# Performance work log

Measured on AMD Instinct MI355X. Metric: run time of the kernel, lower is better.

## Reference

```python
import jax, jax.numpy as jnp
import numpy as np

OUTPUT_SIZE = 512


def _build_schedule(n, m):
    """Static pyramid-circuit schedule of Givens/RBS gates on n wires.

    Sequential gate order (matches theta ordering): for k = 1..n-1, apply
    gates on adjacent wire pairs (i, i+1) for i = k-1 down to max(k-m, 0).
    Total gates = (2n - m - 1) * m // 2. Gates are packed into a brickwork
    schedule (timestep t = 2(k-1) - i) so each layer touches disjoint pairs
    and the whole chain runs in T = n + m - 2 parallel layers.
    Padded slots point at dummy wires (n, n+1) and are masked to identity.
    """
    layers = {}
    t_idx = 0
    for k in range(1, n):
        for i in range(k - 1, max(k - m, 0) - 1, -1):
            t = 2 * (k - 1) - i
            layers.setdefault(t, []).append((i, t_idx))
            t_idx += 1
    T = max(layers) + 1
    W = max(len(v) for v in layers.values())
    wire = np.full((T, W), n, dtype=np.int32)   # pad gates hit dummy wires (n, n+1)
    tidx = np.zeros((T, W), dtype=np.int32)
    mask = np.zeros((T, W), dtype=np.float32)
    for t, gs in layers.items():
        for j, (i, ti) in enumerate(gs):
            wire[t, j] = i
            tidx[t, j] = ti
            mask[t, j] = 1.0
    return wire, tidx, mask


def apply_orthogonal(thetas, x, output_size):
    input_size = x.shape[-1]
    n, m = max(input_size, output_size), min(input_size, output_size)
    wire, tidx, mask = _build_schedule(n, m)
    if input_size < n:
        x = jnp.pad(x, ((0, 0), (0, n - input_size)))
    state = jnp.pad(x, ((0, 0), (0, 2)))          # two dummy columns for padded gate slots
    th = thetas[jnp.asarray(tidx)]                # [T, W]
    msk = jnp.asarray(mask)
    cos = jnp.where(msk > 0, jnp.cos(th), 1.0)    # padded slots -> identity rotation
    sin = jnp.where(msk > 0, jnp.sin(th), 0.0)
    wa = jnp.asarray(wire)                        # [T, W] first wire of each pair
    wb = wa + 1

    def step(st, layer):
        c, s, a_idx, b_idx = layer
        a = st[:, a_idx]                          # [B, W]
        b = st[:, b_idx]
        st = st.at[:, a_idx].set(c * a + s * b)   # RBS rotation on each pair
        st = st.at[:, b_idx].set(c * b - s * a)
        return st, None

    state, _ = jax.lax.scan(step, state, (cos, sin, wa, wb))
    return state[:, :output_size]


def setup_inputs():
    key = jax.random.key(0)
    k1, k2 = jax.random.split(key)
    B, N = 256, 512
    n_thetas = (2 * max(N, OUTPUT_SIZE) - min(N, OUTPUT_SIZE) - 1) * min(N, OUTPUT_SIZE) // 2
    x = jax.random.normal(k1, (B, N), dtype=jnp.float32)
    thetas = jax.random.uniform(k2, (n_thetas,), dtype=jnp.float32,
                                minval=-np.pi, maxval=np.pi)
    bias = jnp.zeros((OUTPUT_SIZE,), dtype=jnp.float32)
    return {"x": x, "thetas": thetas, "bias": bias}


def reference(x, thetas, bias):
    # normalize_inputs=False path; with_bias=True
    out = apply_orthogonal(thetas, x, OUTPUT_SIZE)
    return out + bias
```

## Files before the change

### kernel.cpp

```cpp
#include <hip/hip_runtime.h>
#include <hip/hip_fp16.h>
#include <stdint.h>


#define N_WIRES 512
#define BATCH   256
#define PAIRS   510
#define PF      10
#define FINAL4  (PAIRS * 128)
#define TOTAL4  (FINAL4 + 64)
#define TOTALH2 (TOTAL4 * 4)

__global__ __launch_bounds__(256) void fused_kernel(
    const float* __restrict__ thetas, __half2* __restrict__ Wh) {
  int tid = blockIdx.x * 256 + threadIdx.x;
  if (tid >= TOTALH2) return;
  float c = 1.0f, s = 0.0f;
  if (tid < PAIRS * 512) {
    int p = tid >> 9, r = tid & 511;
    int h = r >> 8, rr = r & 255, L = rr >> 2, j = rr & 3;
    int t = 2 * p + h;
    int i = 8 * L + 2 * j + h;
    if (i <= min(t, 1020 - t)) {
      int k = ((t + i) >> 1) + 1;
      int idx = ((k * (k - 1)) >> 1) + (k - 1 - i);
      __sincosf(thetas[idx], &s, &c);
    }
    if (h == 1 && j == 3) c -= 1.0f;
  } else {
    int e = tid - PAIRS * 512;
    int L = e >> 2, j = e & 3;
    if (8 * L + 2 * j == 0) __sincosf(thetas[130815], &s, &c);
  }
  Wh[tid] = __floats2half2_rn(c, s);
}

template <int N>
__device__ __forceinline__ void wait_vm() {
  asm volatile("s_waitcnt vmcnt(%0)" ::"i"(N) : "memory");
}

__device__ __forceinline__ float dpp_shr1(float v) {
  return __int_as_float(
      __builtin_amdgcn_mov_dpp(__float_as_int(v), 0x138, 0xF, 0xF, true));
}
__device__ __forceinline__ float dpp_shl1(float v) {
  return __int_as_float(
      __builtin_amdgcn_mov_dpp(__float_as_int(v), 0x130, 0xF, 0xF, true));
}
__device__ __forceinline__ uint32_t dpp_shr1_u(uint32_t v) {
  return (uint32_t)__builtin_amdgcn_mov_dpp((int)v, 0x138, 0xF, 0xF, true);
}

__device__ __forceinline__ float mix_s(uint32_t g, float b) {
  float d;
  asm("v_fma_mix_f32 %0, %1, %2, 0 op_sel:[1,0,0] op_sel_hi:[1,0,0]"
      : "=v"(d)
      : "v"(g), "v"(b));
  return d;
}
__device__ __forceinline__ float mix_ns(uint32_t g, float b) {
  float d;
  asm("v_fma_mix_f32 %0, -%1, %2, 0 op_sel:[1,0,0] op_sel_hi:[1,0,0]"
      : "=v"(d)
      : "v"(g), "v"(b));
  return d;
}
__device__ __forceinline__ float mix_c_acc(uint32_t g, float b, float acc) {
  float d;
  asm("v_fma_mix_f32 %0, %1, %2, %3 op_sel:[0,0,0] op_sel_hi:[1,0,0]"
      : "=v"(d)
      : "v"(g), "v"(b), "v"(acc));
  return d;
}

__device__ __forceinline__ void gate_mix(float& a, float& b, uint32_t g) {
  float t = mix_s(g, b);
  float u = mix_ns(g, a);
  float na = mix_c_acc(g, a, t);
  float nb = mix_c_acc(g, b, u);
  a = na;
  b = nb;
}

__device__ __forceinline__ void pair_compute(float& v0, float& v1, float& v2,
                                             float& v3, float& v4, float& v5,
                                             float& v6, float& v7,
                                             const uint4& E, const uint4& O) {
  gate_mix(v0, v1, E.x);
  gate_mix(v2, v3, E.y);
  gate_mix(v4, v5, E.z);
  gate_mix(v6, v7, E.w);
  uint32_t bl = dpp_shr1_u(O.w);
  float rv0 = dpp_shl1(v0);
  float lv7 = dpp_shr1(v7);
  gate_mix(v1, v2, O.x);
  gate_mix(v3, v4, O.y);
  gate_mix(v5, v6, O.z);
  float t = mix_s(O.w, rv0);
  t = mix_c_acc(O.w, v7, t);
  v7 = t + v7;
  float u = mix_ns(bl, lv7);
  u = mix_c_acc(bl, v0, u);
  v0 = u + v0;
}

__global__ __launch_bounds__(64, 1) void circuit_kernel(
    const float* __restrict__ x, const uint32_t* __restrict__ W,
    const float* __restrict__ bias, float* __restrict__ out) {
  const int lane = threadIdx.x;
  const int row = blockIdx.x;
  const uint4* __restrict__ Wg = (const uint4*)W;

  uint4 R[PF][2];
  const uint4* pw = Wg + lane;
#pragma unroll
  for (int s = 0; s < PF; ++s) {
    R[s][0] = pw[0];
    R[s][1] = pw[64];
    pw += 128;
  }

  const float* xr = x + row * N_WIRES + lane * 8;
  float4 x0 = *(const float4*)(xr);
  float4 x1 = *(const float4*)(xr + 4);
  float v0 = x0.x, v1 = x0.y, v2 = x0.z, v3 = x0.w;
  float v4 = x1.x, v5 = x1.y, v6 = x1.z, v7 = x1.w;

  for (int blk = 0; blk < (PAIRS / PF) - 1; ++blk) {
#pragma unroll
    for (int s = 0; s < PF; ++s) {
      wait_vm<18>();
      pair_compute(v0, v1, v2, v3, v4, v5, v6, v7, R[s][0], R[s][1]);
      R[s][0] = pw[0];
      R[s][1] = pw[64];
      pw += 128;
    }
  }

  wait_vm<0>();
#pragma unroll
  for (int s = 0; s < PF; ++s)
    pair_compute(v0, v1, v2, v3, v4, v5, v6, v7, R[s][0], R[s][1]);

  uint4 F = Wg[FINAL4 + lane];
  gate_mix(v0, v1, F.x);
  gate_mix(v2, v3, F.y);
  gate_mix(v4, v5, F.z);
  gate_mix(v6, v7, F.w);

  const float* br = bias + lane * 8;
  float4 b0 = *(const float4*)(br);
  float4 b1 = *(const float4*)(br + 4);
  float* orow = out + row * N_WIRES + lane * 8;
  float4 o0 = {v0 + b0.x, v1 + b0.y, v2 + b0.z, v3 + b0.w};
  float4 o1 = {v4 + b1.x, v5 + b1.y, v6 + b1.z, v7 + b1.w};
  *(float4*)(orow) = o0;
  *(float4*)(orow + 4) = o1;
}

extern "C" void kernel_launch(void* const* d_in, const int* in_sizes, int n_in,
                              void* d_out, int out_size, void* d_ws,
                              size_t ws_size, hipStream_t stream) {
  const float* x = (const float*)d_in[0];
  const float* thetas = (const float*)d_in[1];
  const float* bias = (const float*)d_in[2];
  float* out = (float*)d_out;

  uint32_t* W = (uint32_t*)d_ws;

  fused_kernel<<<(TOTALH2 + 255) / 256, 256, 0, stream>>>(thetas, (__half2*)W);
  circuit_kernel<<<BATCH, 64, 0, stream>>>(x, W, bias, out);
}
```

Measured before the change: 115.5 us.

## Compose gate windows into banded fp16 matrices and apply via MFMA

The per-row sequential simulation of all gate layers is replaced with a two-stage scheme. A window kernel propagates basis vectors through each block of 57 layer-pairs, producing nine banded 512x512 fp16 transfer matrices. The apply kernel then multiplies batches of 16 rows by these matrices with MFMA, using only the three diagonal 64-wide blocks, and ping-pongs the activations in shared memory. This trades the long serial dependency chain for more total arithmetic, converts activations to fp16 (a precision risk), and runs the apply stage on only 16 blocks.

```diff
diff --git a/kernel.cpp b/kernel.cpp
--- a/kernel.cpp
+++ b/kernel.cpp
@@ -3,35 +3,30 @@
 #include <stdint.h>
 
 
-#define N_WIRES 512
-#define BATCH   256
-#define PAIRS   510
-#define PF      10
-#define FINAL4  (PAIRS * 128)
-#define TOTAL4  (FINAL4 + 64)
-#define TOTALH2 (TOTAL4 * 4)
+#define PAIRS   511
+#define TOTALH2 (PAIRS * 512)
+#define NWIN    9
+#define WPAIRS  57
+#define VT_ELEMS (512 * 512)
+#define VT_OFF_BYTES 1048576
+
+typedef _Float16 half8_t __attribute__((ext_vector_type(8)));
+typedef float f32x4_t __attribute__((ext_vector_type(4)));
 
 __global__ __launch_bounds__(256) void fused_kernel(
     const float* __restrict__ thetas, __half2* __restrict__ Wh) {
   int tid = blockIdx.x * 256 + threadIdx.x;
-  if (tid >= TOTALH2) return;
+  int p = tid >> 9, r = tid & 511;
+  int h = r >> 8, rr = r & 255, L = rr >> 2, j = rr & 3;
+  int t = 2 * p + h;
+  int i = 8 * L + 2 * j + h;
   float c = 1.0f, s = 0.0f;
-  if (tid < PAIRS * 512) {
-    int p = tid >> 9, r = tid & 511;
-    int h = r >> 8, rr = r & 255, L = rr >> 2, j = rr & 3;
-    int t = 2 * p + h;
-    int i = 8 * L + 2 * j + h;
-    if (i <= min(t, 1020 - t)) {
-      int k = ((t + i) >> 1) + 1;
-      int idx = ((k * (k - 1)) >> 1) + (k - 1 - i);
-      __sincosf(thetas[idx], &s, &c);
-    }
-    if (h == 1 && j == 3) c -= 1.0f;
-  } else {
-    int e = tid - PAIRS * 512;
-    int L = e >> 2, j = e & 3;
-    if (8 * L + 2 * j == 0) __sincosf(thetas[130815], &s, &c);
-  }
+  if (i <= min(t, 1020 - t)) {
+    int k = ((t + i) >> 1) + 1;
+    int idx = ((k * (k - 1)) >> 1) + (k - 1 - i);
+    __sincosf(thetas[idx], &s, &c);
+  }
+  if (h == 1 && j == 3) c -= 1.0f;
   Wh[tid] = __floats2half2_rn(c, s);
 }
 
@@ -39,41 +34,33 @@
 __device__ __forceinline__ void wait_vm() {
   asm volatile("s_waitcnt vmcnt(%0)" ::"i"(N) : "memory");
 }
-
-__device__ __forceinline__ float dpp_shr1(float v) {
+template <int CTRL>
+__device__ __forceinline__ float dpp_f(float v) {
   return __int_as_float(
-      __builtin_amdgcn_mov_dpp(__float_as_int(v), 0x138, 0xF, 0xF, true));
-}
-__device__ __forceinline__ float dpp_shl1(float v) {
-  return __int_as_float(
-      __builtin_amdgcn_mov_dpp(__float_as_int(v), 0x130, 0xF, 0xF, true));
-}
-__device__ __forceinline__ uint32_t dpp_shr1_u(uint32_t v) {
-  return (uint32_t)__builtin_amdgcn_mov_dpp((int)v, 0x138, 0xF, 0xF, true);
-}
-
+      __builtin_amdgcn_mov_dpp(__float_as_int(v), CTRL, 0xF, 0xF, true));
+}
+template <int CTRL>
+__device__ __forceinline__ uint32_t dpp_u(uint32_t v) {
+  return (uint32_t)__builtin_amdgcn_mov_dpp((int)v, CTRL, 0xF, 0xF, true);
+}
 __device__ __forceinline__ float mix_s(uint32_t g, float b) {
   float d;
   asm("v_fma_mix_f32 %0, %1, %2, 0 op_sel:[1,0,0] op_sel_hi:[1,0,0]"
-      : "=v"(d)
-      : "v"(g), "v"(b));
+      : "=v"(d) : "v"(g), "v"(b));
   return d;
 }
 __device__ __forceinline__ float mix_ns(uint32_t g, float b) {
   float d;
   asm("v_fma_mix_f32 %0, -%1, %2, 0 op_sel:[1,0,0] op_sel_hi:[1,0,0]"
-      : "=v"(d)
-      : "v"(g), "v"(b));
+      : "=v"(d) : "v"(g), "v"(b));
   return d;
 }
 __device__ __forceinline__ float mix_c_acc(uint32_t g, float b, float acc) {
   float d;
   asm("v_fma_mix_f32 %0, %1, %2, %3 op_sel:[0,0,0] op_sel_hi:[1,0,0]"
-      : "=v"(d)
-      : "v"(g), "v"(b), "v"(acc));
+      : "=v"(d) : "v"(g), "v"(b), "v"(acc));
   return d;
 }
-
 __device__ __forceinline__ void gate_mix(float& a, float& b, uint32_t g) {
   float t = mix_s(g, b);
   float u = mix_ns(g, a);
@@ -83,6 +70,7 @@
   b = nb;
 }
 
+template <int CSHL, int CSHR>
 __device__ __forceinline__ void pair_compute(float& v0, float& v1, float& v2,
                                              float& v3, float& v4, float& v5,
                                              float& v6, float& v7,
@@ -91,9 +79,9 @@
   gate_mix(v2, v3, E.y);
   gate_mix(v4, v5, E.z);
   gate_mix(v6, v7, E.w);
-  uint32_t bl = dpp_shr1_u(O.w);
-  float rv0 = dpp_shl1(v0);
-  float lv7 = dpp_shr1(v7);
+  uint32_t bl = dpp_u<CSHR>(O.w);
+  float rv0 = dpp_f<CSHL>(v0);
+  float lv7 = dpp_f<CSHR>(v7);
   gate_mix(v1, v2, O.x);
   gate_mix(v3, v4, O.y);
   gate_mix(v5, v6, O.z);
@@ -105,58 +93,144 @@
   v0 = u + v0;
 }
 
-__global__ __launch_bounds__(64, 1) void circuit_kernel(
-    const float* __restrict__ x, const uint32_t* __restrict__ W,
+__global__ __launch_bounds__(64) void window_kernel(
+    const uint32_t* __restrict__ W, _Float16* __restrict__ VT) {
+  const int lane = threadIdx.x;
+  const int gl = lane & 15, grp = lane >> 4;
+  const int w = blockIdx.x >> 7;
+  const int d = ((blockIdx.x & 127) << 2) + grp;
+  int b0 = d - 58;
+  int base = (b0 <= 0) ? 0 : (b0 & ~7);
+  base = min(base, 384);
+  const int idx0 = (base >> 3) + gl;
+  const int wire0 = base + 8 * gl;
+
+  float v0 = (wire0 + 0 == d) ? 1.f : 0.f;
+  float v1 = (wire0 + 1 == d) ? 1.f : 0.f;
+  float v2 = (wire0 + 2 == d) ? 1.f : 0.f;
+  float v3 = (wire0 + 3 == d) ? 1.f : 0.f;
+  float v4 = (wire0 + 4 == d) ? 1.f : 0.f;
+  float v5 = (wire0 + 5 == d) ? 1.f : 0.f;
+  float v6 = (wire0 + 6 == d) ? 1.f : 0.f;
+  float v7 = (wire0 + 7 == d) ? 1.f : 0.f;
+
+  const int p0 = w * WPAIRS;
+  const int p1 = min(PAIRS, p0 + WPAIRS);
+  const uint4* __restrict__ Wg = (const uint4*)W;
+
+  uint4 R[4][2];
+#pragma unroll
+  for (int s0 = 0; s0 < 4; ++s0) {
+    int p = min(p0 + s0, p1 - 1);
+    R[s0][0] = Wg[p * 128 + idx0];
+    R[s0][1] = Wg[p * 128 + 64 + idx0];
+  }
+  for (int p = p0; p < p1; ++p) {
+    int s = (p - p0) & 3;
+    wait_vm<6>();
+    pair_compute<0x101, 0x111>(v0, v1, v2, v3, v4, v5, v6, v7, R[s][0], R[s][1]);
+    int pn = min(p + 4, p1 - 1);
+    R[s][0] = Wg[pn * 128 + idx0];
+    R[s][1] = Wg[pn * 128 + 64 + idx0];
+  }
+
+  _Float16* vtw = VT + (size_t)w * VT_ELEMS + d;
+  const int q = d >> 6;
+  const int c0 = max(0, q - 1) << 6;
+  const int c1 = (min(7, q + 1) << 6) + 64;
+  vtw[(size_t)(wire0 + 0) * 512] = (_Float16)v0;
+  vtw[(size_t)(wire0 + 1) * 512] = (_Float16)v1;
+  vtw[(size_t)(wire0 + 2) * 512] = (_Float16)v2;
+  vtw[(size_t)(wire0 + 3) * 512] = (_Float16)v3;
+  vtw[(size_t)(wire0 + 4) * 512] = (_Float16)v4;
+  vtw[(size_t)(wire0 + 5) * 512] = (_Float16)v5;
+  vtw[(size_t)(wire0 + 6) * 512] = (_Float16)v6;
+  vtw[(size_t)(wire0 + 7) * 512] = (_Float16)v7;
+  for (int c = c0 + gl; c < base; c += 16)
+    vtw[(size_t)c * 512] = (_Float16)0.f;
+  for (int c = base + 128 + gl; c < c1; c += 16)
+    vtw[(size_t)c * 512] = (_Float16)0.f;
+}
+
+__global__ __launch_bounds__(256, 1) void apply_kernel(
+    const float* __restrict__ x, const _Float16* __restrict__ VT,
     const float* __restrict__ bias, float* __restrict__ out) {
-  const int lane = threadIdx.x;
-  const int row = blockIdx.x;
-  const uint4* __restrict__ Wg = (const uint4*)W;
-
-  uint4 R[PF][2];
-  const uint4* pw = Wg + lane;
-#pragma unroll
-  for (int s = 0; s < PF; ++s) {
-    R[s][0] = pw[0];
-    R[s][1] = pw[64];
-    pw += 128;
-  }
-
-  const float* xr = x + row * N_WIRES + lane * 8;
-  float4 x0 = *(const float4*)(xr);
-  float4 x1 = *(const float4*)(xr + 4);
-  float v0 = x0.x, v1 = x0.y, v2 = x0.z, v3 = x0.w;
-  float v4 = x1.x, v5 = x1.y, v6 = x1.z, v7 = x1.w;
-
-  for (int blk = 0; blk < (PAIRS / PF) - 1; ++blk) {
-#pragma unroll
-    for (int s = 0; s < PF; ++s) {
-      wait_vm<18>();
-      pair_compute(v0, v1, v2, v3, v4, v5, v6, v7, R[s][0], R[s][1]);
-      R[s][0] = pw[0];
-      R[s][1] = pw[64];
-      pw += 128;
+  __shared__ float S0[16 * 516];
+  __shared__ float S1[16 * 516];
+  const int tid = threadIdx.x;
+  const int lane = tid & 63;
+  const int wv = tid >> 6;
+  const int r16 = lane & 15;
+  const int h = lane >> 4;
+  const float* xb = x + blockIdx.x * (16 * 512);
+
+#pragma unroll
+  for (int i = 0; i < 8; ++i) {
+    int e = tid + i * 256;
+    int r = e >> 7, cq = e & 127;
+    float4 t = ((const float4*)xb)[e];
+    *(float4*)&S0[r * 516 + cq * 4] = t;
+  }
+  __syncthreads();
+
+  for (int w = 0; w < NWIN; ++w) {
+    const float* cur = (w & 1) ? S1 : S0;
+    float* nxt = (w & 1) ? S0 : S1;
+    const _Float16* vtw = VT + (size_t)w * VT_ELEMS;
+#pragma unroll
+    for (int ti = 0; ti < 2; ++ti) {
+      const int n = wv * 2 + ti;
+      f32x4_t acc0 = {0.f, 0.f, 0.f, 0.f};
+      f32x4_t acc1 = acc0, acc2 = acc0, acc3 = acc0;
+#pragma unroll
+      for (int kbr = 0; kbr < 3; ++kbr) {
+        const int kb = n + kbr - 1;
+        if (kb >= 0 && kb <= 7) {
+#pragma unroll
+          for (int ks = 0; ks < 2; ++ks) {
+            const int koff = kb * 64 + ks * 32 + h * 8;
+            const float* ap = cur + r16 * 516 + koff;
+            float4 a0 = *(const float4*)(ap);
+            float4 a1 = *(const float4*)(ap + 4);
+            half8_t af;
+            af[0] = (_Float16)a0.x; af[1] = (_Float16)a0.y;
+            af[2] = (_Float16)a0.z; af[3] = (_Float16)a0.w;
+            af[4] = (_Float16)a1.x; af[5] = (_Float16)a1.y;
+            af[6] = (_Float16)a1.z; af[7] = (_Float16)a1.w;
+            const _Float16* bp = vtw + (size_t)(n * 64 + r16) * 512 + koff;
+            half8_t b0 = *(const half8_t*)(bp);
+            half8_t b1 = *(const half8_t*)(bp + (size_t)16 * 512);
+            half8_t b2 = *(const half8_t*)(bp + (size_t)32 * 512);
+            half8_t b3 = *(const half8_t*)(bp + (size_t)48 * 512);
+            acc0 = __builtin_amdgcn_mfma_f32_16x16x32_f16(af, b0, acc0, 0, 0, 0);
+            acc1 = __builtin_amdgcn_mfma_f32_16x16x32_f16(af, b1, acc1, 0, 0, 0);
+            acc2 = __builtin_amdgcn_mfma_f32_16x16x32_f16(af, b2, acc2, 0, 0, 0);
+            acc3 = __builtin_amdgcn_mfma_f32_16x16x32_f16(af, b3, acc3, 0, 0, 0);
+          }
+        }
+      }
+      const int cb = n * 64 + r16;
+#pragma unroll
+      for (int jj = 0; jj < 4; ++jj) {
+        nxt[(4 * h + jj) * 516 + cb + 0]  = acc0[jj];
+        nxt[(4 * h + jj) * 516 + cb + 16] = acc1[jj];
+        nxt[(4 * h + jj) * 516 + cb + 32] = acc2[jj];
+        nxt[(4 * h + jj) * 516 + cb + 48] = acc3[jj];
+      }
     }
-  }
-
-  wait_vm<0>();
-#pragma unroll
-  for (int s = 0; s < PF; ++s)
-    pair_compute(v0, v1, v2, v3, v4, v5, v6, v7, R[s][0], R[s][1]);
-
-  uint4 F = Wg[FINAL4 + lane];
-  gate_mix(v0, v1, F.x);
-  gate_mix(v2, v3, F.y);
-  gate_mix(v4, v5, F.z);
-  gate_mix(v6, v7, F.w);
-
-  const float* br = bias + lane * 8;
-  float4 b0 = *(const float4*)(br);
-  float4 b1 = *(const float4*)(br + 4);
-  float* orow = out + row * N_WIRES + lane * 8;
-  float4 o0 = {v0 + b0.x, v1 + b0.y, v2 + b0.z, v3 + b0.w};
-  float4 o1 = {v4 + b1.x, v5 + b1.y, v6 + b1.z, v7 + b1.w};
-  *(float4*)(orow) = o0;
-  *(float4*)(orow + 4) = o1;
+    __syncthreads();
+  }
+
+  float* ob = out + blockIdx.x * (16 * 512);
+#pragma unroll
+  for (int i = 0; i < 8; ++i) {
+    int e = tid + i * 256;
+    int r = e >> 7, cq = e & 127;
+    float4 t = *(const float4*)&S1[r * 516 + cq * 4];
+    float4 bv = ((const float4*)bias)[cq];
+    float4 o = {t.x + bv.x, t.y + bv.y, t.z + bv.z, t.w + bv.w};
+    ((float4*)ob)[e] = o;
+  }
 }
 
 extern "C" void kernel_launch(void* const* d_in, const int* in_sizes, int n_in,
@@ -168,7 +242,9 @@
   float* out = (float*)d_out;
 
   uint32_t* W = (uint32_t*)d_ws;
-
-  fused_kernel<<<(TOTALH2 + 255) / 256, 256, 0, stream>>>(thetas, (__half2*)W);
-  circuit_kernel<<<BATCH, 64, 0, stream>>>(x, W, bias, out);
-}
+  _Float16* VT = (_Float16*)((char*)d_ws + VT_OFF_BYTES);
+
+  fused_kernel<<<TOTALH2 / 256, 256, 0, stream>>>(thetas, (__half2*)W);
+  window_kernel<<<NWIN * 128, 64, 0, stream>>>((const uint32_t*)W, VT);
+  apply_kernel<<<16, 256, 0, stream>>>(x, VT, bias, out);
+}
```

Result: slower. 141.9 us (+22.8%).
